# Kernel tuning notes

Measured on AMD Instinct MI355X. Metric: run time of the kernel, lower is better.

Reference implementation:

```python
import jax, jax.numpy as jnp
import numpy as np

D_MODEL = 1024
NHEAD = 16
HEAD_DIM = D_MODEL // NHEAD
B, T = 2, 2048


def setup_inputs() -> dict:
    key = jax.random.key(0)
    ks = jax.random.split(key, 11)
    s = 1.0 / np.sqrt(D_MODEL)
    inp = {
        'q': jax.random.normal(ks[0], (B, T, D_MODEL), jnp.float32),
        'k': jax.random.normal(ks[1], (B, T, D_MODEL), jnp.float32),
        'v': jax.random.normal(ks[2], (B, T, D_MODEL), jnp.float32),
        'Wq': jax.random.normal(ks[3], (D_MODEL, D_MODEL), jnp.float32) * s,
        'bq': jnp.zeros((D_MODEL,), jnp.float32),
        'Wk': jax.random.normal(ks[4], (D_MODEL, D_MODEL), jnp.float32) * s,
        'bk': jnp.zeros((D_MODEL,), jnp.float32),
        'Wv': jax.random.normal(ks[5], (D_MODEL, D_MODEL), jnp.float32) * s,
        'bv': jnp.zeros((D_MODEL,), jnp.float32),
        'Wo': jax.random.normal(ks[6], (D_MODEL, D_MODEL), jnp.float32) * s,
        'bo': jnp.zeros((D_MODEL,), jnp.float32),
    }
    return inp


def reference(q, k, v, Wq, bq, Wk, bk, Wv, bv, Wo, bo):
    scale = np.sqrt(HEAD_DIM).astype(np.float32)
    # projections (torch Linear: x @ W.T + b), split heads -> [B, H, T, Dh]
    def proj(x, W, b):
        y = jnp.einsum('btd,ed->bte', x, W) + b
        return y.reshape(B, T, NHEAD, HEAD_DIM).transpose(0, 2, 1, 3)
    qh = proj(q, Wq, bq)
    kh = proj(k, Wk, bk)
    vh = proj(v, Wv, bv)
    scores = jnp.einsum('bhqd,bhkd->bhqk', qh, kh) / scale  # [B,H,T,T]
    weights = jax.nn.softmax(scores, axis=-1)
    out = jnp.einsum('bhqk,bhkd->bhqd', weights, vh)        # [B,H,T,Dh]
    out = out.transpose(0, 2, 1, 3).reshape(B, T, D_MODEL)
    return jnp.einsum('btd,ed->bte', out, Wo) + bo
```

## Files before the change

kernel.cpp:

```cpp
#include <hip/hip_runtime.h>
#include <cstdint>
#include <cstddef>


#define D_MODEL 1024
#define NHEAD   16
#define HDIM    64
#define BATCH   2
#define SEQ     2048
#define BT      (BATCH * SEQ)

typedef __bf16 bf16;
typedef __bf16 bf16x8 __attribute__((ext_vector_type(8)));
typedef __bf16 bf16x4 __attribute__((ext_vector_type(4)));
typedef float  floatx4 __attribute__((ext_vector_type(4)));

#define MFMA16(a, b, c) __builtin_amdgcn_mfma_f32_16x16x32_bf16((a), (b), (c), 0, 0, 0)

__device__ __forceinline__ void async_cp16(const bf16* g, bf16* l) {
  __builtin_amdgcn_global_load_lds(
      (__attribute__((address_space(1))) void*)(g),
      (__attribute__((address_space(3))) void*)(l), 16, 0, 0);
}

__global__ __launch_bounds__(256) void cvt7(
    const float* __restrict__ s0, const float* __restrict__ s1,
    const float* __restrict__ s2, const float* __restrict__ s3,
    const float* __restrict__ s4, const float* __restrict__ s5,
    const float* __restrict__ s6,
    bf16* __restrict__ d0, bf16* __restrict__ d1, bf16* __restrict__ d2,
    bf16* __restrict__ d3, bf16* __restrict__ d4, bf16* __restrict__ d5,
    bf16* __restrict__ d6)
{
  const float* src; bf16* dst; int n4;
  switch (blockIdx.y) {
    case 0:  src = s0; dst = d0; n4 = (BT * D_MODEL) / 4; break;
    case 1:  src = s1; dst = d1; n4 = (BT * D_MODEL) / 4; break;
    case 2:  src = s2; dst = d2; n4 = (BT * D_MODEL) / 4; break;
    case 3:  src = s3; dst = d3; n4 = (D_MODEL * D_MODEL) / 4; break;
    case 4:  src = s4; dst = d4; n4 = (D_MODEL * D_MODEL) / 4; break;
    case 5:  src = s5; dst = d5; n4 = (D_MODEL * D_MODEL) / 4; break;
    default: src = s6; dst = d6; n4 = (D_MODEL * D_MODEL) / 4; break;
  }
  int stride = gridDim.x * blockDim.x;
  for (int i = blockIdx.x * blockDim.x + threadIdx.x; i < n4; i += stride) {
    float4 f = ((const float4*)src)[i];
    bf16x4 h;
    h[0] = (bf16)f.x; h[1] = (bf16)f.y; h[2] = (bf16)f.z; h[3] = (bf16)f.w;
    ((bf16x4*)dst)[i] = h;
  }
}

__device__ __forceinline__ void gemm128_core(
    const bf16* __restrict__ A, const bf16* __restrict__ W,
    int m0, int n0, bf16* As, bf16* Bs, floatx4 acc[4][4])
{
  const int t = threadIdx.x;
  const int l = t & 63, w = t >> 6;
  const int quad = l >> 4, lr = l & 15;
  const int wm = (w >> 1) * 64, wn = (w & 1) * 64;

  floatx4 z = {0.f, 0.f, 0.f, 0.f};
#pragma unroll
  for (int i = 0; i < 4; i++)
#pragma unroll
    for (int j = 0; j < 4; j++) acc[i][j] = z;

  for (int kt = 0; kt < 1024; kt += 32) {
    __syncthreads();
#pragma unroll
    for (int i = 0; i < 2; i++) {
      int c = i * 256 + t;
      int row = c >> 2, ci = c & 3;
      async_cp16(A + (size_t)(m0 + row) * 1024 + kt + ci * 8,
                 As + (i * 256 + w * 64) * 8);
      async_cp16(W + (size_t)(n0 + row) * 1024 + kt + ci * 8,
                 Bs + (i * 256 + w * 64) * 8);
    }
    __syncthreads();

    bf16x8 af[4], bfr[4];
#pragma unroll
    for (int i = 0; i < 4; i++) {
      af[i]  = *(const bf16x8*)(As + (wm + i * 16 + lr) * 32 + quad * 8);
      bfr[i] = *(const bf16x8*)(Bs + (wn + i * 16 + lr) * 32 + quad * 8);
    }
#pragma unroll
    for (int i = 0; i < 4; i++)
#pragma unroll
      for (int j = 0; j < 4; j++)
        acc[i][j] = MFMA16(af[i], bfr[j], acc[i][j]);
  }
}

__global__ __launch_bounds__(256) void qkv_gemm(
    const bf16* __restrict__ qb, const bf16* __restrict__ kb, const bf16* __restrict__ vb,
    const bf16* __restrict__ wq, const bf16* __restrict__ wk, const bf16* __restrict__ wv,
    const float* __restrict__ biasq, const float* __restrict__ biask, const float* __restrict__ biasv,
    bf16* __restrict__ qh, bf16* __restrict__ kh, bf16* __restrict__ vt)
{
  __shared__ bf16 As[128 * 32];
  __shared__ bf16 Bs[128 * 32];
  const int zid = blockIdx.z;
  const bf16* A = (zid == 0) ? qb : ((zid == 1) ? kb : vb);
  const bf16* W = (zid == 0) ? wq : ((zid == 1) ? wk : wv);
  const float* bias = (zid == 0) ? biasq : ((zid == 1) ? biask : biasv);
  const int m0 = blockIdx.x * 128, n0 = blockIdx.y * 128;

  floatx4 acc[4][4];
  gemm128_core(A, W, m0, n0, As, Bs, acc);

  const int t = threadIdx.x, l = t & 63, w = t >> 6;
  const int quad = l >> 4, lr = l & 15;
  const int wm = (w >> 1) * 64, wn = (w & 1) * 64;

  if (zid < 2) {
    bf16* out = (zid == 0) ? qh : kh;
#pragma unroll
    for (int i = 0; i < 4; i++) {
      int mbase = m0 + wm + i * 16 + quad * 4;
      int b  = mbase >> 11;
      int tq = mbase & 2047;
#pragma unroll
      for (int j = 0; j < 4; j++) {
        int n = n0 + wn + j * 16 + lr;
        float bv = bias[n];
        int h = n >> 6, dh = n & 63;
        bf16* p = out + ((size_t)((b * NHEAD + h) * SEQ + tq)) * HDIM + dh;
#pragma unroll
        for (int r = 0; r < 4; r++)
          p[(size_t)r * HDIM] = (bf16)(acc[i][j][r] + bv);
      }
    }
  } else {
#pragma unroll
    for (int i = 0; i < 4; i++) {
      int mbase = m0 + wm + i * 16 + quad * 4;
      int b  = mbase >> 11;
      int tq = mbase & 2047;
#pragma unroll
      for (int j = 0; j < 4; j++) {
        int n = n0 + wn + j * 16 + lr;
        float bv = bias[n];
        int h = n >> 6, dh = n & 63;
        bf16x4 pk;
#pragma unroll
        for (int r = 0; r < 4; r++) pk[r] = (bf16)(acc[i][j][r] + bv);
        *(bf16x4*)(vt + ((size_t)((b * NHEAD + h) * HDIM + dh)) * SEQ + tq) = pk;
      }
    }
  }
}

__global__ __launch_bounds__(512, 4) void attn_fused(
    const bf16* __restrict__ qh, const bf16* __restrict__ kh,
    const bf16* __restrict__ vt, bf16* __restrict__ attn)
{
  __shared__ bf16 Ks[128 * 72];
  __shared__ bf16 Vts[64 * 136];
  __shared__ bf16 Pbuf[8 * 16 * 40];

  const int t = threadIdx.x, l = t & 63, w = t >> 6;
  const int quad = l >> 4, lr = l & 15;
  const int bh = blockIdx.y;
  const int qt0 = blockIdx.x * 128;
  const bf16* qg = qh + (size_t)bh * SEQ * HDIM;
  const bf16* kg = kh + (size_t)bh * SEQ * HDIM;
  const bf16* vg = vt + (size_t)bh * HDIM * SEQ;

  bf16x8 qf[2];
#pragma unroll
  for (int ko = 0; ko < 2; ko++)
    qf[ko] = *(const bf16x8*)(qg + (size_t)(qt0 + w * 16 + lr) * HDIM
                              + ko * 32 + quad * 8);

  floatx4 zz = {0.f, 0.f, 0.f, 0.f};
  floatx4 Oacc[4];
#pragma unroll
  for (int di = 0; di < 4; di++) Oacc[di] = zz;
  float mrow = -3.0e38f, lrow = 0.f;
  const float scale = 0.125f;

  bf16* pw = Pbuf + w * 16 * 40;

  for (int kt0 = 0; kt0 < SEQ; kt0 += 128) {
    __syncthreads();
#pragma unroll
    for (int i = 0; i < 2; i++) {
      int c = t + 512 * i;
      { int row = c >> 3, ci = c & 7;
        *(int4*)(Ks + row * 72 + ci * 8) =
            *(const int4*)(kg + (size_t)(kt0 + row) * HDIM + ci * 8); }
      { int row = c >> 4, ci = c & 15;
        *(int4*)(Vts + row * 136 + ci * 8) =
            *(const int4*)(vg + (size_t)row * SEQ + kt0 + ci * 8); }
    }
    __syncthreads();

    floatx4 s[8];
#pragma unroll
    for (int ni = 0; ni < 8; ni++) {
      bf16x8 k0 = *(const bf16x8*)(Ks + (ni * 16 + lr) * 72 + quad * 8);
      bf16x8 k1 = *(const bf16x8*)(Ks + (ni * 16 + lr) * 72 + 32 + quad * 8);
      floatx4 a = zz;
      a = MFMA16(k0, qf[0], a);
      a = MFMA16(k1, qf[1], a);
      s[ni] = a;
    }

    float rmax = s[0][0];
#pragma unroll
    for (int ni = 0; ni < 8; ni++)
#pragma unroll
      for (int r = 0; r < 4; r++) rmax = fmaxf(rmax, s[ni][r]);
    rmax = fmaxf(rmax, __shfl_xor(rmax, 16, 64));
    rmax = fmaxf(rmax, __shfl_xor(rmax, 32, 64));

    float mnew  = fmaxf(mrow, rmax * scale);
    float alpha = __expf(mrow - mnew);
    mrow = mnew;

    float rsum = 0.f;
#pragma unroll
    for (int ni = 0; ni < 8; ni++)
#pragma unroll
      for (int r = 0; r < 4; r++) {
        float pv = __expf(s[ni][r] * scale - mnew);
        s[ni][r] = pv;
        rsum += pv;
      }
    rsum += __shfl_xor(rsum, 16, 64);
    rsum += __shfl_xor(rsum, 32, 64);
    lrow = lrow * alpha + rsum;

    float am[4];
#pragma unroll
    for (int r = 0; r < 4; r++)
      am[r] = __shfl(alpha, (l & 48) | (quad * 4 + r), 64);
#pragma unroll
    for (int di = 0; di < 4; di++)
#pragma unroll
      for (int r = 0; r < 4; r++) Oacc[di][r] *= am[r];

#pragma unroll
    for (int kk = 0; kk < 4; kk++) {
#pragma unroll
      for (int jj = 0; jj < 2; jj++) {
        int ni = kk * 2 + jj;
        bf16x4 pk;
#pragma unroll
        for (int r = 0; r < 4; r++) pk[r] = (bf16)s[ni][r];
        *(bf16x4*)(pw + lr * 40 + jj * 16 + quad * 4) = pk;
      }
      bf16x8 pa = *(const bf16x8*)(pw + lr * 40 + quad * 8);
#pragma unroll
      for (int di = 0; di < 4; di++) {
        bf16x8 vfr = *(const bf16x8*)(Vts + (di * 16 + lr) * 136 + kk * 32 + quad * 8);
        Oacc[di] = MFMA16(pa, vfr, Oacc[di]);
      }
    }
  }

  float inv = 1.0f / lrow;
  float im[4];
#pragma unroll
  for (int r = 0; r < 4; r++)
    im[r] = __shfl(inv, (l & 48) | (quad * 4 + r), 64);
  const int b = bh >> 4, h = bh & 15;
#pragma unroll
  for (int di = 0; di < 4; di++)
#pragma unroll
    for (int r = 0; r < 4; r++) {
      int tq = qt0 + w * 16 + quad * 4 + r;
      attn[((size_t)b * SEQ + tq) * D_MODEL + h * HDIM + di * 16 + lr] =
          (bf16)(Oacc[di][r] * im[r]);
    }
}

__global__ __launch_bounds__(256) void oproj_gemm(
    const bf16* __restrict__ attn, const bf16* __restrict__ wo,
    const float* __restrict__ bo, float* __restrict__ out)
{
  __shared__ bf16 As[128 * 32];
  __shared__ bf16 Bs[128 * 32];
  const int m0 = blockIdx.x * 128, n0 = blockIdx.y * 128;

  floatx4 acc[4][4];
  gemm128_core(attn, wo, m0, n0, As, Bs, acc);

  const int t = threadIdx.x, l = t & 63, w = t >> 6;
  const int quad = l >> 4, lr = l & 15;
  const int wm = (w >> 1) * 64, wn = (w & 1) * 64;

#pragma unroll
  for (int i = 0; i < 4; i++) {
    int m = m0 + wm + i * 16 + quad * 4;
#pragma unroll
    for (int j = 0; j < 4; j++) {
      int n = n0 + wn + j * 16 + lr;
      float bv = bo[n];
      float* p = out + (size_t)m * D_MODEL + n;
#pragma unroll
      for (int r = 0; r < 4; r++)
        p[(size_t)r * D_MODEL] = acc[i][j][r] + bv;
    }
  }
}

extern "C" void kernel_launch(void* const* d_in, const int* in_sizes, int n_in,
                              void* d_out, int out_size, void* d_ws, size_t ws_size,
                              hipStream_t stream)
{
  const float* q  = (const float*)d_in[0];
  const float* k  = (const float*)d_in[1];
  const float* v  = (const float*)d_in[2];
  const float* Wq = (const float*)d_in[3];
  const float* bq = (const float*)d_in[4];
  const float* Wk = (const float*)d_in[5];
  const float* bk = (const float*)d_in[6];
  const float* Wv = (const float*)d_in[7];
  const float* bv = (const float*)d_in[8];
  const float* Wo = (const float*)d_in[9];
  const float* bo = (const float*)d_in[10];

  const size_t NQ = (size_t)BT * D_MODEL;
  const size_t NW = (size_t)D_MODEL * D_MODEL;

  bf16* p = (bf16*)d_ws;
  bf16* qb   = p; p += NQ;
  bf16* kb   = p; p += NQ;
  bf16* vb   = p; p += NQ;
  bf16* wqb  = p; p += NW;
  bf16* wkb  = p; p += NW;
  bf16* wvb  = p; p += NW;
  bf16* wob  = p; p += NW;
  bf16* qhp  = p; p += NQ;
  bf16* khp  = p; p += NQ;
  bf16* vtp  = p; p += NQ;
  bf16* attn = p; p += NQ;

  cvt7<<<dim3(1024, 7, 1), 256, 0, stream>>>(q, k, v, Wq, Wk, Wv, Wo,
                                             qb, kb, vb, wqb, wkb, wvb, wob);
  qkv_gemm<<<dim3(32, 8, 3), 256, 0, stream>>>(qb, kb, vb, wqb, wkb, wvb,
                                               bq, bk, bv, qhp, khp, vtp);
  attn_fused<<<dim3(16, 32, 1), 512, 0, stream>>>(qhp, khp, vtp, attn);
  oproj_gemm<<<dim3(32, 8, 1), 256, 0, stream>>>(attn, wob, bo, (float*)d_out);
}
```

Before: 241.2 us.

## Split attention keys across wave halves, keep P in registers, merge partial softmax

The attention kernel now assigns each wave 32 query rows and half of each 128-key tile, so each K fragment loaded from LDS is reused across two query tiles. P stays in registers and feeds a 16x16x16 MFMA with V as the A operand, which removes the per-wave LDS round trip for P. The two halves' partial (max, sum, O) are combined through shared memory at the end, and the output is staged in LDS so it can be written to global memory with coalesced 16-byte stores. This adds an end-of-kernel reduction, extra barriers and larger LDS use, and the smaller-K MFMA issues more instructions for the PV product.

```diff
diff --git a/kernel.cpp b/kernel.cpp
--- a/kernel.cpp
+++ b/kernel.cpp
@@ -14,8 +14,14 @@
 typedef __bf16 bf16x8 __attribute__((ext_vector_type(8)));
 typedef __bf16 bf16x4 __attribute__((ext_vector_type(4)));
 typedef float  floatx4 __attribute__((ext_vector_type(4)));
+typedef short  short4v __attribute__((ext_vector_type(4)));
 
 #define MFMA16(a, b, c) __builtin_amdgcn_mfma_f32_16x16x32_bf16((a), (b), (c), 0, 0, 0)
+
+__device__ __forceinline__ floatx4 MFMA16B(bf16x4 a, bf16x4 b, floatx4 c) {
+  return __builtin_amdgcn_mfma_f32_16x16x16bf16_1k(
+      __builtin_bit_cast(short4v, a), __builtin_bit_cast(short4v, b), c, 0, 0, 0);
+}
 
 __device__ __forceinline__ void async_cp16(const bf16* g, bf16* l) {
   __builtin_amdgcn_global_load_lds(
@@ -156,32 +162,36 @@
     const bf16* __restrict__ qh, const bf16* __restrict__ kh,
     const bf16* __restrict__ vt, bf16* __restrict__ attn)
 {
-  __shared__ bf16 Ks[128 * 72];
-  __shared__ bf16 Vts[64 * 136];
-  __shared__ bf16 Pbuf[8 * 16 * 40];
+  __shared__ __align__(16) char smem[55296];
+  bf16* Ks  = (bf16*)smem;
+  bf16* Vts = (bf16*)(smem + 18432);
+  bf16* Ost = (bf16*)(smem + 36864);
 
   const int t = threadIdx.x, l = t & 63, w = t >> 6;
   const int quad = l >> 4, lr = l & 15;
+  const int qsel = w & 3, half = w >> 2;
   const int bh = blockIdx.y;
   const int qt0 = blockIdx.x * 128;
   const bf16* qg = qh + (size_t)bh * SEQ * HDIM;
   const bf16* kg = kh + (size_t)bh * SEQ * HDIM;
   const bf16* vg = vt + (size_t)bh * HDIM * SEQ;
 
-  bf16x8 qf[2];
-#pragma unroll
-  for (int ko = 0; ko < 2; ko++)
-    qf[ko] = *(const bf16x8*)(qg + (size_t)(qt0 + w * 16 + lr) * HDIM
-                              + ko * 32 + quad * 8);
+  bf16x8 qf[2][2];
+#pragma unroll
+  for (int qt = 0; qt < 2; qt++)
+#pragma unroll
+    for (int ko = 0; ko < 2; ko++)
+      qf[qt][ko] = *(const bf16x8*)(qg + (size_t)(qt0 + qsel * 32 + qt * 16 + lr) * HDIM
+                                    + ko * 32 + quad * 8);
 
   floatx4 zz = {0.f, 0.f, 0.f, 0.f};
-  floatx4 Oacc[4];
-#pragma unroll
-  for (int di = 0; di < 4; di++) Oacc[di] = zz;
-  float mrow = -3.0e38f, lrow = 0.f;
+  floatx4 Oacc[4][2];
+#pragma unroll
+  for (int dt = 0; dt < 4; dt++)
+#pragma unroll
+    for (int qt = 0; qt < 2; qt++) Oacc[dt][qt] = zz;
+  float mrow[2] = {-3.0e38f, -3.0e38f}, lrow[2] = {0.f, 0.f};
   const float scale = 0.125f;
-
-  bf16* pw = Pbuf + w * 16 * 40;
 
   for (int kt0 = 0; kt0 < SEQ; kt0 += 128) {
     __syncthreads();
@@ -197,84 +207,114 @@
     }
     __syncthreads();
 
-    floatx4 s[8];
-#pragma unroll
-    for (int ni = 0; ni < 8; ni++) {
-      bf16x8 k0 = *(const bf16x8*)(Ks + (ni * 16 + lr) * 72 + quad * 8);
-      bf16x8 k1 = *(const bf16x8*)(Ks + (ni * 16 + lr) * 72 + 32 + quad * 8);
-      floatx4 a = zz;
-      a = MFMA16(k0, qf[0], a);
-      a = MFMA16(k1, qf[1], a);
-      s[ni] = a;
-    }
-
-    float rmax = s[0][0];
-#pragma unroll
-    for (int ni = 0; ni < 8; ni++)
-#pragma unroll
-      for (int r = 0; r < 4; r++) rmax = fmaxf(rmax, s[ni][r]);
-    rmax = fmaxf(rmax, __shfl_xor(rmax, 16, 64));
-    rmax = fmaxf(rmax, __shfl_xor(rmax, 32, 64));
-
-    float mnew  = fmaxf(mrow, rmax * scale);
-    float alpha = __expf(mrow - mnew);
-    mrow = mnew;
-
-    float rsum = 0.f;
-#pragma unroll
-    for (int ni = 0; ni < 8; ni++)
-#pragma unroll
-      for (int r = 0; r < 4; r++) {
-        float pv = __expf(s[ni][r] * scale - mnew);
-        s[ni][r] = pv;
-        rsum += pv;
-      }
-    rsum += __shfl_xor(rsum, 16, 64);
-    rsum += __shfl_xor(rsum, 32, 64);
-    lrow = lrow * alpha + rsum;
-
-    float am[4];
-#pragma unroll
-    for (int r = 0; r < 4; r++)
-      am[r] = __shfl(alpha, (l & 48) | (quad * 4 + r), 64);
-#pragma unroll
-    for (int di = 0; di < 4; di++)
-#pragma unroll
-      for (int r = 0; r < 4; r++) Oacc[di][r] *= am[r];
-
-#pragma unroll
-    for (int kk = 0; kk < 4; kk++) {
-#pragma unroll
-      for (int jj = 0; jj < 2; jj++) {
-        int ni = kk * 2 + jj;
-        bf16x4 pk;
-#pragma unroll
-        for (int r = 0; r < 4; r++) pk[r] = (bf16)s[ni][r];
-        *(bf16x4*)(pw + lr * 40 + jj * 16 + quad * 4) = pk;
-      }
-      bf16x8 pa = *(const bf16x8*)(pw + lr * 40 + quad * 8);
-#pragma unroll
-      for (int di = 0; di < 4; di++) {
-        bf16x8 vfr = *(const bf16x8*)(Vts + (di * 16 + lr) * 136 + kk * 32 + quad * 8);
-        Oacc[di] = MFMA16(pa, vfr, Oacc[di]);
-      }
-    }
-  }
-
-  float inv = 1.0f / lrow;
-  float im[4];
-#pragma unroll
-  for (int r = 0; r < 4; r++)
-    im[r] = __shfl(inv, (l & 48) | (quad * 4 + r), 64);
+    floatx4 s[4][2];
+#pragma unroll
+    for (int kt = 0; kt < 4; kt++) {
+      const bf16* krow = Ks + (half * 64 + kt * 16 + lr) * 72 + quad * 8;
+      bf16x8 a0 = *(const bf16x8*)(krow);
+      bf16x8 a1 = *(const bf16x8*)(krow + 32);
+#pragma unroll
+      for (int qt = 0; qt < 2; qt++) {
+        floatx4 a = zz;
+        a = MFMA16(a0, qf[qt][0], a);
+        a = MFMA16(a1, qf[qt][1], a);
+        s[kt][qt] = a;
+      }
+    }
+
+    bf16x4 pk[4][2];
+    float al[2];
+#pragma unroll
+    for (int qt = 0; qt < 2; qt++) {
+      float rmax = s[0][qt][0];
+#pragma unroll
+      for (int kt = 0; kt < 4; kt++)
+#pragma unroll
+        for (int r = 0; r < 4; r++) rmax = fmaxf(rmax, s[kt][qt][r]);
+      rmax = fmaxf(rmax, __shfl_xor(rmax, 16, 64));
+      rmax = fmaxf(rmax, __shfl_xor(rmax, 32, 64));
+      float mnew = fmaxf(mrow[qt], rmax * scale);
+      al[qt] = __expf(mrow[qt] - mnew);
+      mrow[qt] = mnew;
+      float rsum = 0.f;
+#pragma unroll
+      for (int kt = 0; kt < 4; kt++)
+#pragma unroll
+        for (int r = 0; r < 4; r++) {
+          float pv = __expf(s[kt][qt][r] * scale - mnew);
+          rsum += pv;
+          pk[kt][qt][r] = (bf16)pv;
+        }
+      rsum += __shfl_xor(rsum, 16, 64);
+      rsum += __shfl_xor(rsum, 32, 64);
+      lrow[qt] = lrow[qt] * al[qt] + rsum;
+#pragma unroll
+      for (int dt = 0; dt < 4; dt++)
+#pragma unroll
+        for (int r = 0; r < 4; r++) Oacc[dt][qt][r] *= al[qt];
+    }
+
+#pragma unroll
+    for (int kt = 0; kt < 4; kt++)
+#pragma unroll
+      for (int dt = 0; dt < 4; dt++) {
+        bf16x4 vf = *(const bf16x4*)(Vts + (dt * 16 + lr) * 136
+                                     + half * 64 + kt * 16 + quad * 4);
+#pragma unroll
+        for (int qt = 0; qt < 2; qt++)
+          Oacc[dt][qt] = MFMA16B(vf, pk[kt][qt], Oacc[dt][qt]);
+      }
+  }
+
+  __syncthreads();
+
+  if (half == 1) {
+#pragma unroll
+    for (int qt = 0; qt < 2; qt++) {
+#pragma unroll
+      for (int dt = 0; dt < 4; dt++) {
+        int tid = (qsel * 2 + qt) * 4 + dt;
+        *(floatx4*)(smem + tid * 1024 + l * 16) = Oacc[dt][qt];
+      }
+      if (quad == 0)
+        *(float2*)(smem + 32768 + ((qsel * 2 + qt) * 16 + lr) * 8) =
+            make_float2(mrow[qt], lrow[qt]);
+    }
+  }
+  __syncthreads();
+
+  if (half == 0) {
+#pragma unroll
+    for (int qt = 0; qt < 2; qt++) {
+      float2 st = *(const float2*)(smem + 32768 + ((qsel * 2 + qt) * 16 + lr) * 8);
+      float ms = fmaxf(mrow[qt], st.x);
+      float aA = __expf(mrow[qt] - ms);
+      float aB = __expf(st.x - ms);
+      float inv = 1.0f / (lrow[qt] * aA + st.y * aB);
+      float fA = aA * inv, fB = aB * inv;
+#pragma unroll
+      for (int dt = 0; dt < 4; dt++) {
+        int tid = (qsel * 2 + qt) * 4 + dt;
+        floatx4 ob = *(const floatx4*)(smem + tid * 1024 + l * 16);
+        int qloc = qsel * 32 + qt * 16 + lr;
+        bf16x4 ov;
+#pragma unroll
+        for (int r = 0; r < 4; r++)
+          ov[r] = (bf16)(Oacc[dt][qt][r] * fA + ob[r] * fB);
+        *(bf16x4*)(Ost + qloc * 72 + dt * 16 + quad * 4) = ov;
+      }
+    }
+  }
+  __syncthreads();
+
   const int b = bh >> 4, h = bh & 15;
 #pragma unroll
-  for (int di = 0; di < 4; di++)
-#pragma unroll
-    for (int r = 0; r < 4; r++) {
-      int tq = qt0 + w * 16 + quad * 4 + r;
-      attn[((size_t)b * SEQ + tq) * D_MODEL + h * HDIM + di * 16 + lr] =
-          (bf16)(Oacc[di][r] * im[r]);
-    }
+  for (int i = 0; i < 2; i++) {
+    int c = t + 512 * i;
+    int row = c >> 3, ci = c & 7;
+    *(int4*)(attn + ((size_t)b * SEQ + qt0 + row) * D_MODEL + h * HDIM + ci * 8) =
+        *(const int4*)(Ost + row * 72 + ci * 8);
+  }
 }
 
 __global__ __launch_bounds__(256) void oproj_gemm(
```

Measured after the change: 255.1 us. +5.8%, slower.

## Keep P in registers via transposed 16x16x16 MFMA and stage output through LDS

Applied to the files above, without the earlier changes.

The attention kernel now computes O^T = V^T·P^T with the 16x16x16 bf16 MFMA, so the softmax probabilities feed the MFMA directly from registers. This removes the per-wave LDS round-trip for P and the cross-lane shuffles of alpha and 1/l, since each lane now owns a whole query column. The epilogue writes the output tile to LDS, which reuses the K/V space, and then issues coalesced 16-byte global stores instead of scattered 2-byte stores. The trade-off is twice as many MFMA instructions, each with half the K depth, plus narrower 8-byte V reads from LDS.

```diff
diff --git a/kernel.cpp b/kernel.cpp
--- a/kernel.cpp
+++ b/kernel.cpp
@@ -14,8 +14,14 @@
 typedef __bf16 bf16x8 __attribute__((ext_vector_type(8)));
 typedef __bf16 bf16x4 __attribute__((ext_vector_type(4)));
 typedef float  floatx4 __attribute__((ext_vector_type(4)));
+typedef short  short4v __attribute__((ext_vector_type(4)));
 
 #define MFMA16(a, b, c) __builtin_amdgcn_mfma_f32_16x16x32_bf16((a), (b), (c), 0, 0, 0)
+
+__device__ __forceinline__ floatx4 MFMA16B(bf16x4 a, bf16x4 b, floatx4 c) {
+  return __builtin_amdgcn_mfma_f32_16x16x16bf16_1k(
+      __builtin_bit_cast(short4v, a), __builtin_bit_cast(short4v, b), c, 0, 0, 0);
+}
 
 __device__ __forceinline__ void async_cp16(const bf16* g, bf16* l) {
   __builtin_amdgcn_global_load_lds(
@@ -156,9 +162,10 @@
     const bf16* __restrict__ qh, const bf16* __restrict__ kh,
     const bf16* __restrict__ vt, bf16* __restrict__ attn)
 {
-  __shared__ bf16 Ks[128 * 72];
-  __shared__ bf16 Vts[64 * 136];
-  __shared__ bf16 Pbuf[8 * 16 * 40];
+  __shared__ __align__(16) char smem[35840];
+  bf16* Ks  = (bf16*)smem;
+  bf16* Vts = (bf16*)(smem + 18432);
+  bf16* Ost = (bf16*)smem;
 
   const int t = threadIdx.x, l = t & 63, w = t >> 6;
   const int quad = l >> 4, lr = l & 15;
@@ -177,11 +184,9 @@
   floatx4 zz = {0.f, 0.f, 0.f, 0.f};
   floatx4 Oacc[4];
 #pragma unroll
-  for (int di = 0; di < 4; di++) Oacc[di] = zz;
+  for (int dt = 0; dt < 4; dt++) Oacc[dt] = zz;
   float mrow = -3.0e38f, lrow = 0.f;
   const float scale = 0.125f;
-
-  bf16* pw = Pbuf + w * 16 * 40;
 
   for (int kt0 = 0; kt0 < SEQ; kt0 += 128) {
     __syncthreads();
@@ -200,8 +205,9 @@
     floatx4 s[8];
 #pragma unroll
     for (int ni = 0; ni < 8; ni++) {
-      bf16x8 k0 = *(const bf16x8*)(Ks + (ni * 16 + lr) * 72 + quad * 8);
-      bf16x8 k1 = *(const bf16x8*)(Ks + (ni * 16 + lr) * 72 + 32 + quad * 8);
+      const bf16* krow = Ks + (ni * 16 + lr) * 72 + quad * 8;
+      bf16x8 k0 = *(const bf16x8*)(krow);
+      bf16x8 k1 = *(const bf16x8*)(krow + 32);
       floatx4 a = zz;
       a = MFMA16(k0, qf[0], a);
       a = MFMA16(k1, qf[1], a);
@@ -215,66 +221,57 @@
       for (int r = 0; r < 4; r++) rmax = fmaxf(rmax, s[ni][r]);
     rmax = fmaxf(rmax, __shfl_xor(rmax, 16, 64));
     rmax = fmaxf(rmax, __shfl_xor(rmax, 32, 64));
-
-    float mnew  = fmaxf(mrow, rmax * scale);
-    float alpha = __expf(mrow - mnew);
+    float mnew = fmaxf(mrow, rmax * scale);
+    float al = __expf(mrow - mnew);
     mrow = mnew;
 
+    bf16x4 pk[8];
     float rsum = 0.f;
 #pragma unroll
     for (int ni = 0; ni < 8; ni++)
 #pragma unroll
       for (int r = 0; r < 4; r++) {
         float pv = __expf(s[ni][r] * scale - mnew);
-        s[ni][r] = pv;
         rsum += pv;
+        pk[ni][r] = (bf16)pv;
       }
     rsum += __shfl_xor(rsum, 16, 64);
     rsum += __shfl_xor(rsum, 32, 64);
-    lrow = lrow * alpha + rsum;
-
-    float am[4];
-#pragma unroll
-    for (int r = 0; r < 4; r++)
-      am[r] = __shfl(alpha, (l & 48) | (quad * 4 + r), 64);
-#pragma unroll
-    for (int di = 0; di < 4; di++)
-#pragma unroll
-      for (int r = 0; r < 4; r++) Oacc[di][r] *= am[r];
-
-#pragma unroll
-    for (int kk = 0; kk < 4; kk++) {
-#pragma unroll
-      for (int jj = 0; jj < 2; jj++) {
-        int ni = kk * 2 + jj;
-        bf16x4 pk;
-#pragma unroll
-        for (int r = 0; r < 4; r++) pk[r] = (bf16)s[ni][r];
-        *(bf16x4*)(pw + lr * 40 + jj * 16 + quad * 4) = pk;
+    lrow = lrow * al + rsum;
+#pragma unroll
+    for (int dt = 0; dt < 4; dt++)
+#pragma unroll
+      for (int r = 0; r < 4; r++) Oacc[dt][r] *= al;
+
+#pragma unroll
+    for (int ni = 0; ni < 8; ni++)
+#pragma unroll
+      for (int dt = 0; dt < 4; dt++) {
+        bf16x4 vf = *(const bf16x4*)(Vts + (dt * 16 + lr) * 136
+                                     + ni * 16 + quad * 4);
+        Oacc[dt] = MFMA16B(vf, pk[ni], Oacc[dt]);
       }
-      bf16x8 pa = *(const bf16x8*)(pw + lr * 40 + quad * 8);
-#pragma unroll
-      for (int di = 0; di < 4; di++) {
-        bf16x8 vfr = *(const bf16x8*)(Vts + (di * 16 + lr) * 136 + kk * 32 + quad * 8);
-        Oacc[di] = MFMA16(pa, vfr, Oacc[di]);
-      }
-    }
   }
 
   float inv = 1.0f / lrow;
-  float im[4];
-#pragma unroll
-  for (int r = 0; r < 4; r++)
-    im[r] = __shfl(inv, (l & 48) | (quad * 4 + r), 64);
+  __syncthreads();
+#pragma unroll
+  for (int dt = 0; dt < 4; dt++) {
+    bf16x4 ov;
+#pragma unroll
+    for (int r = 0; r < 4; r++) ov[r] = (bf16)(Oacc[dt][r] * inv);
+    *(bf16x4*)(Ost + (size_t)(w * 16 + lr) * 72 + dt * 16 + quad * 4) = ov;
+  }
+  __syncthreads();
+
   const int b = bh >> 4, h = bh & 15;
 #pragma unroll
-  for (int di = 0; di < 4; di++)
-#pragma unroll
-    for (int r = 0; r < 4; r++) {
-      int tq = qt0 + w * 16 + quad * 4 + r;
-      attn[((size_t)b * SEQ + tq) * D_MODEL + h * HDIM + di * 16 + lr] =
-          (bf16)(Oacc[di][r] * im[r]);
-    }
+  for (int i = 0; i < 2; i++) {
+    int c = t + 512 * i;
+    int row = c >> 3, ci = c & 7;
+    *(int4*)(attn + ((size_t)b * SEQ + qt0 + row) * D_MODEL + h * HDIM + ci * 8) =
+        *(const int4*)(Ost + row * 72 + ci * 8);
+  }
 }
 
 __global__ __launch_bounds__(256) void oproj_gemm(
```

Measured after the change: 238.6 us. Within noise of the previous version (-1.1%).
